# Kernel optimization log

Measured on AMD Instinct MI355X. Metric: run time of the kernel, lower is better.

The kernel has to match this reference:

```python
import jax, jax.numpy as jnp
import numpy as np

N_NODES = 10000
N_EDGES = 128000


def _edge_conv(x, row, col, edge_attr, w1, b1, w2, b2):
    # gather endpoints, concat edge features, 2-layer MLP per edge
    m = jnp.concatenate([x[row], x[col], edge_attr], axis=1)  # [E, 2*in+edge]
    m = jax.nn.relu(m @ w1 + b1) @ w2 + b2                    # [E, out]
    # scatter-mean onto source nodes (flow='target_to_source' -> aggregate on row)
    n = x.shape[0]
    s = jax.ops.segment_sum(m, row, num_segments=n)
    cnt = jax.ops.segment_sum(jnp.ones((row.shape[0], 1), m.dtype), row, num_segments=n)
    out = s / jnp.maximum(cnt, 1.0)
    return out, m


def setup_inputs() -> dict:
    key = jax.random.key(0)
    ks = jax.random.split(key, 24)
    f = jnp.float32

    def lin(kw, kb, fan_in, fan_out):
        lim = 1.0 / np.sqrt(fan_in)
        w = jax.random.uniform(kw, (fan_in, fan_out), f, -lim, lim)
        b = jax.random.uniform(kb, (fan_out,), f, -lim, lim)
        return w, b

    inp = {}
    inp['x_org'] = jax.random.normal(ks[0], (N_NODES, 256), f)
    inp['x_rot'] = jax.random.normal(ks[1], (N_NODES, 4), f)
    inp['edge_index'] = jax.random.randint(ks[2], (2, N_EDGES), 0, N_NODES, jnp.int64 if jax.config.jax_enable_x64 else jnp.int32)
    inp['edge_attr'] = jax.random.normal(ks[3], (N_EDGES, 640), f)
    inp['edge_rot'] = jax.random.normal(ks[4], (N_EDGES, 4), f)

    # conv1: Linear(2*260+644=1164, 64), Linear(64, 64)
    inp['c1_w1'], inp['c1_b1'] = lin(ks[5], ks[6], 1164, 64)
    inp['c1_w2'], inp['c1_b2'] = lin(ks[7], ks[8], 64, 64)
    # conv2: Linear(2*64+704=832, 64), Linear(64, 64)
    inp['c2_w1'], inp['c2_b1'] = lin(ks[9], ks[10], 832, 64)
    inp['c2_w2'], inp['c2_b2'] = lin(ks[11], ks[12], 64, 64)
    # conv3: Linear(2*128+128=384, 64), Linear(64, 64)
    inp['c3_w1'], inp['c3_b1'] = lin(ks[13], ks[14], 384, 64)
    inp['c3_w2'], inp['c3_b2'] = lin(ks[15], ks[16], 64, 64)
    # conv4: Linear(384, 64), Linear(64, 64)
    inp['c4_w1'], inp['c4_b1'] = lin(ks[17], ks[18], 384, 64)
    inp['c4_w2'], inp['c4_b2'] = lin(ks[19], ks[20], 64, 64)
    # lin1: Linear(64, 4)
    inp['lin1_w'], inp['lin1_b'] = lin(ks[21], ks[22], 64, 4)
    # edge_fc: Linear(64, 32) -> ReLU -> Linear(32, 1)
    k23 = jax.random.split(ks[23], 4)
    inp['efc_w1'], inp['efc_b1'] = lin(k23[0], k23[1], 64, 32)
    inp['efc_w2'], inp['efc_b2'] = lin(k23[2], k23[3], 32, 1)
    return inp


def reference(x_org, x_rot, edge_index, edge_attr, edge_rot,
              c1_w1, c1_b1, c1_w2, c1_b2,
              c2_w1, c2_b1, c2_w2, c2_b2,
              c3_w1, c3_b1, c3_w2, c3_b2,
              c4_w1, c4_b1, c4_w2, c4_b2,
              lin1_w, lin1_b, efc_w1, efc_b1, efc_w2, efc_b2):
    node_feat = jnp.concatenate([x_org, x_rot], axis=1)
    edge_feat = jnp.concatenate([edge_attr, edge_rot], axis=1)
    row, col = edge_index[0], edge_index[1]
    E = edge_index.shape[1]

    x1, edge_x1 = _edge_conv(node_feat, row, col, edge_feat, c1_w1, c1_b1, c1_w2, c1_b2)
    edge_x1 = jax.nn.relu(edge_x1)

    x2, edge_x2 = _edge_conv(x1, row, col, jnp.concatenate([edge_attr, edge_x1], axis=1),
                             c2_w1, c2_b1, c2_w2, c2_b2)
    x2 = jax.nn.relu(x2)
    edge_x2 = jax.nn.relu(edge_x2)

    x3, edge_x3 = _edge_conv(jnp.concatenate([x2, x1], axis=1), row, col,
                             jnp.concatenate([edge_x2, edge_x1], axis=1),
                             c3_w1, c3_b1, c3_w2, c3_b2)
    x3 = jax.nn.relu(x3)
    edge_x3 = jax.nn.relu(edge_x3)

    x4, edge_x4 = _edge_conv(jnp.concatenate([x3, x2], axis=1), row, col,
                             jnp.concatenate([edge_x3, edge_x2], axis=1),
                             c4_w1, c4_b1, c4_w2, c4_b2)
    x4 = jax.nn.relu(x4)

    x = x4 @ lin1_w + lin1_b  # [N, 4]
    h = edge_x4[: E // 2] + edge_x4[E // 2:]
    pred_edge_res = jax.nn.relu(h @ efc_w1 + efc_b1) @ efc_w2 + efc_b2  # [E/2, 1]

    # F.normalize(x, p=2, dim=1)
    x = x / jnp.maximum(jnp.linalg.norm(x, axis=1, keepdims=True), 1e-12)
    return x, pred_edge_res
```

## Files before the change

### kernel.cpp

```cpp
#include <hip/hip_runtime.h>
#include <stdint.h>


#define N_NODES 10000
#define N_EDGES 128000
#define E_HALF  64000
#define NBLK    1000

typedef unsigned short u16;

using bf16x8 = __attribute__((ext_vector_type(8))) short;
using f32x4  = __attribute__((ext_vector_type(4))) float;

#define MFMA16(A, B, C) C = __builtin_amdgcn_mfma_f32_16x16x32_bf16(A, B, C, 0, 0, 0)

__device__ __align__(256) float g_acc[N_NODES * 64];
__device__ __align__(256) float g_deg[N_NODES];
__device__ __align__(256) float g_P[N_NODES * 128];
__device__ __align__(256) float g_x1[N_NODES * 64];
__device__ __align__(256) float g_x2[N_NODES * 64];
__device__ __align__(256) float g_x3[N_NODES * 64];
__device__ __align__(256) u16  g_fragA[(size_t)NBLK * 16384];
__device__ __align__(256) u16  g_fragB[(size_t)NBLK * 16384];
__device__ __align__(256) float g_Q2 [(size_t)NBLK * 8192];
__device__ __align__(256) float g_ex4[(size_t)N_EDGES * 64];
__device__ __align__(256) u16  g_wpA_hi[5 * 4096];
__device__ __align__(256) u16  g_wpA_lo[5 * 4096];
__device__ __align__(256) u16  g_wp2_hi[4 * 4096];
__device__ __align__(256) u16  g_wp2_lo[4 * 4096];
__device__ __align__(256) u16  g_wnp_hi[9 * 8192];
__device__ __align__(256) u16  g_wnp_lo[9 * 8192];
__device__ __align__(256) u16  g_wpC_hi[10 * 8192];
__device__ __align__(256) u16  g_wpC_lo[10 * 8192];
__device__ __align__(256) int g_row[N_EDGES];
__device__ __align__(256) int g_col[N_EDGES];
__device__ int g_mode;
__device__ int g_is64;

__device__ __forceinline__ float b2f(u16 u) {
    return __uint_as_float(((unsigned int)u) << 16);
}
__device__ __forceinline__ u16 f2b(float f) {
    unsigned int u = __float_as_uint(f);
    u += 0x7FFFu + ((u >> 16) & 1u);
    return (u16)(u >> 16);
}
__device__ __forceinline__ float ldf(const u16* p)   { return b2f(*p); }
__device__ __forceinline__ float ldf(const float* p) { return *p; }
__device__ __forceinline__ void  stf(u16* p, float v)   { *p = f2b(v); }
__device__ __forceinline__ void  stf(float* p, float v) { *p = v; }

__device__ __forceinline__ float4 load4(const float* p) { return *(const float4*)p; }
__device__ __forceinline__ float4 load4(const u16* p) {
    ushort4 v = *(const ushort4*)p;
    return make_float4(b2f(v.x), b2f(v.y), b2f(v.z), b2f(v.w));
}

__device__ __forceinline__ void gl_lds16(const void* g, void* l) {
    __builtin_amdgcn_global_load_lds(
        (const __attribute__((address_space(1))) void*)g,
        (__attribute__((address_space(3))) void*)l, 16, 0, 0);
}

__device__ __forceinline__ void split_pack(float4 v, uint2& hi, uint2& lo) {
    unsigned int ux = __float_as_uint(v.x), uy = __float_as_uint(v.y);
    unsigned int uz = __float_as_uint(v.z), uw = __float_as_uint(v.w);
    unsigned int hx = ux & 0xFFFF0000u, hy = uy & 0xFFFF0000u;
    unsigned int hz = uz & 0xFFFF0000u, hw = uw & 0xFFFF0000u;
    hi.x = (hx >> 16) | hy;
    hi.y = (hz >> 16) | hw;
    u16 lx = f2b(v.x - __uint_as_float(hx));
    u16 ly = f2b(v.y - __uint_as_float(hy));
    u16 lz = f2b(v.z - __uint_as_float(hz));
    u16 lw = f2b(v.w - __uint_as_float(hw));
    lo.x = (unsigned int)lx | ((unsigned int)ly << 16);
    lo.y = (unsigned int)lz | ((unsigned int)lw << 16);
}

__device__ __forceinline__ void mk_frag(float4 v0, float4 v1,
                                        bf16x8& fh, bf16x8& fl) {
    uint2 h0, l0, h1, l1;
    split_pack(v0, h0, l0);
    split_pack(v1, h1, l1);
    union { unsigned int w[4]; bf16x8 v; } H, L;
    H.w[0] = h0.x; H.w[1] = h0.y; H.w[2] = h1.x; H.w[3] = h1.y;
    L.w[0] = l0.x; L.w[1] = l0.y; L.w[2] = l1.x; L.w[3] = l1.y;
    fh = H.v; fl = L.v;
}

__global__ void prologue_a(const void* x_org_v, const int* __restrict__ eidx) {
    const int i = blockIdx.x * 256 + threadIdx.x;
    g_acc[i] = 0.f;
    if (i < N_NODES) g_deg[i] = 0.f;
    if (blockIdx.x == 0 && threadIdx.x < 64) {
        const u16* w = (const u16*)x_org_v;
        const int t = threadIdx.x;
        int ok = 0;
        for (int j = t; j < 128; j += 64) {
            u16 v = w[j];
            int ex = (v >> 7) & 0xFF;
            ok += ((ex >= 0x68 && ex <= 0x88) || ((v & 0x7FFFu) == 0)) ? 1 : 0;
        }
        #pragma unroll
        for (int off = 32; off >= 1; off >>= 1) ok += __shfl_xor(ok, off);
        bool allz = true;
        for (int j = t; j < 2048; j += 64) allz = allz && (eidx[2 * j + 1] == 0);
        unsigned long long m = __ballot(allz);
        if (t == 0) {
            g_mode = (ok >= 110) ? 0 : 1;
            g_is64 = (m == ~0ull) ? 1 : 0;
        }
    }
}

__device__ __forceinline__ void pack_pair(u16* dh, u16* dl, float v) {
    const u16 hh = f2b(v);
    *dh = hh; *dl = f2b(v - b2f(hh));
}
template<typename TW>
__device__ void pack_wnp(const TW* w, int hioff, int rem, u16* dh, u16* dl) {
    const int s = rem >> 13, kt = (rem >> 12) & 1, ct = (rem >> 9) & 7,
              l = (rem >> 3) & 63, r = rem & 7;
    const int k = s * 64 + kt * 32 + 4 * (l >> 4) + (r & 3) + 16 * (r >> 2);
    const int col = ct * 16 + (l & 15);
    const int row = (col < 64) ? k : (hioff + k);
    pack_pair(dh + rem, dl + rem, ldf(w + (size_t)row * 64 + (col & 63)));
}
template<typename TW>
__device__ void pack_wpa(const TW* w, int we, int rem, u16* dh, u16* dl) {
    const int s = rem >> 12, kt = (rem >> 11) & 1, ct = (rem >> 9) & 3,
              l = (rem >> 3) & 63, r = rem & 7;
    const int k = s * 64 + kt * 32 + 4 * (l >> 4) + (r & 3) + 16 * (r >> 2);
    pack_pair(dh + rem, dl + rem,
              ldf(w + (size_t)(we + k) * 64 + ct * 16 + (l & 15)));
}
template<typename TW>
__device__ void pack_wpc(const TW* w1, const TW* w2w, int rem) {
    const int s = rem >> 13, kt = (rem >> 12) & 1, ct = (rem >> 9) & 7,
              l = (rem >> 3) & 63, r = rem & 7;
    const int k = s * 64 + kt * 32 + 4 * (l >> 4) + (r & 3) + 16 * (r >> 2);
    const int col = ct * 16 + (l & 15);
    float v = (col < 64) ? ldf(w1 + (size_t)(520 + k) * 64 + col)
                         : ldf(w2w + (size_t)(128 + k) * 64 + (col - 64));
    pack_pair(g_wpC_hi + rem, g_wpC_lo + rem, v);
}

template<typename TW>
__device__ void pack_all_body(const TW* c1w1, const TW* c1w2, const TW* c2w1,
        const TW* c2w2, const TW* c3w1, const TW* c3w2, const TW* c4w1,
        const TW* c4w2) {
    const int idx = blockIdx.x * 256 + threadIdx.x;
    if (idx < 81920)        pack_wpc<TW>(c1w1, c2w1, idx);
    else if (idx < 114688)  pack_wnp<TW>(c1w1, 260, idx - 81920,  g_wnp_hi,            g_wnp_lo);
    else if (idx < 122880)  pack_wnp<TW>(c2w1, 64,  idx - 114688, g_wnp_hi + 4 * 8192, g_wnp_lo + 4 * 8192);
    else if (idx < 139264)  pack_wnp<TW>(c3w1, 128, idx - 122880, g_wnp_hi + 5 * 8192, g_wnp_lo + 5 * 8192);
    else if (idx < 155648)  pack_wnp<TW>(c4w1, 128, idx - 139264, g_wnp_hi + 7 * 8192, g_wnp_lo + 7 * 8192);
    else if (idx < 159744)  pack_wpa<TW>(c2w1, 768, idx - 155648, g_wpA_hi,            g_wpA_lo);
    else if (idx < 167936)  pack_wpa<TW>(c3w1, 256, idx - 159744, g_wpA_hi + 4096,     g_wpA_lo + 4096);
    else if (idx < 176128)  pack_wpa<TW>(c4w1, 256, idx - 167936, g_wpA_hi + 12288,    g_wpA_lo + 12288);
    else if (idx < 180224)  pack_wpa<TW>(c1w2, 0,   idx - 176128, g_wp2_hi,            g_wp2_lo);
    else if (idx < 184320)  pack_wpa<TW>(c2w2, 0,   idx - 180224, g_wp2_hi + 4096,     g_wp2_lo + 4096);
    else if (idx < 188416)  pack_wpa<TW>(c3w2, 0,   idx - 184320, g_wp2_hi + 8192,     g_wp2_lo + 8192);
    else if (idx < 192512)  pack_wpa<TW>(c4w2, 0,   idx - 188416, g_wp2_hi + 12288,    g_wp2_lo + 12288);
}

__global__ void prep_k(const void* c1w1, const void* c1w2, const void* c2w1,
        const void* c2w2, const void* c3w1, const void* c3w2, const void* c4w1,
        const void* c4w2, const int* __restrict__ eidx) {
    if ((int)blockIdx.x < 752) {
        if (g_mode == 0)
            pack_all_body<u16>((const u16*)c1w1, (const u16*)c1w2, (const u16*)c2w1,
                (const u16*)c2w2, (const u16*)c3w1, (const u16*)c3w2,
                (const u16*)c4w1, (const u16*)c4w2);
        else
            pack_all_body<float>((const float*)c1w1, (const float*)c1w2,
                (const float*)c2w1, (const float*)c2w2, (const float*)c3w1,
                (const float*)c3w2, (const float*)c4w1, (const float*)c4w2);
    } else {
        const int e = ((int)blockIdx.x - 752) * 256 + threadIdx.x;
        int row, col;
        if (g_is64) { row = eidx[2 * e]; col = eidx[2 * (e + N_EDGES)]; }
        else        { row = eidx[e];     col = eidx[e + N_EDGES]; }
        g_row[e] = row; g_col[e] = col;
        atomicAdd(&g_deg[row], 1.0f);
    }
}

template<typename TA>
__device__ void node_mfma_in_body(float* smrot, float* smwt,
        const TA* A1, const TA* rotsrc, const TA* w1, float* P) {
    const int t = threadIdx.x;
    const int lane = t & 63, wid = t >> 6;
    const int q = lane >> 4, n = lane & 15;
    const int r0b = blockIdx.x * 64;

    if (t < 64) {
        const int rr = min(r0b + t, N_NODES - 1);
        float4 v = load4(rotsrc + (size_t)rr * 4);
        smrot[t * 4 + 0] = v.x; smrot[t * 4 + 1] = v.y;
        smrot[t * 4 + 2] = v.z; smrot[t * 4 + 3] = v.w;
    }
    for (int i = t; i < 512; i += 256) {
        const int j = i >> 7, c = i & 127;
        const int row = (c < 64) ? (256 + j) : (516 + j);
        smwt[i] = ldf(w1 + (size_t)row * 64 + (c & 63));
    }
    __syncthreads();

    const int arow = min(r0b + wid * 16 + n, N_NODES - 1);

    f32x4 acc[8];
    #pragma unroll
    for (int ct = 0; ct < 8; ++ct) acc[ct] = (f32x4){0.f, 0.f, 0.f, 0.f};

    #pragma unroll
    for (int s = 0; s < 4; ++s) {
        #pragma unroll
        for (int kt = 0; kt < 2; ++kt) {
            const TA* p = A1 + (size_t)arow * 256 + s * 64 + kt * 32 + q * 4;
            float4 v0 = load4(p), v1 = load4(p + 16);
            bf16x8 ah, al;
            mk_frag(v0, v1, ah, al);
            const u16* wph = g_wnp_hi + s * 8192;
            const u16* wpl = g_wnp_lo + s * 8192;
            #pragma unroll
            for (int ct = 0; ct < 8; ++ct) {
                bf16x8 bh = *(const bf16x8*)&wph[(kt * 8 + ct) * 512 + lane * 8];
                bf16x8 bl = *(const bf16x8*)&wpl[(kt * 8 + ct) * 512 + lane * 8];
                MFMA16(ah, bh, acc[ct]);
                MFMA16(al, bh, acc[ct]);
                MFMA16(ah, bl, acc[ct]);
            }
        }
    }

    #pragma unroll
    for (int ct = 0; ct < 8; ++ct) {
        #pragma unroll
        for (int i = 0; i < 4; ++i) {
            const int rl = wid * 16 + 4 * q + i;
            const int row = r0b + rl;
            const int col = ct * 16 + n;
            float v = acc[ct][i]
                    + smrot[rl * 4 + 0] * smwt[0 * 128 + col]
                    + smrot[rl * 4 + 1] * smwt[1 * 128 + col]
                    + smrot[rl * 4 + 2] * smwt[2 * 128 + col]
                    + smrot[rl * 4 + 3] * smwt[3 * 128 + col];
            if (row < N_NODES) P[(size_t)row * 128 + col] = v;
        }
    }
}

__global__ void __launch_bounds__(256) node_mfma_in(
        const void* A1, const void* rotsrc, const void* w1, float* __restrict__ P) {
    __shared__ float smrot[256], smwt[512];
    if (g_mode == 0)
        node_mfma_in_body<u16>(smrot, smwt, (const u16*)A1, (const u16*)rotsrc,
                               (const u16*)w1, P);
    else
        node_mfma_in_body<float>(smrot, smwt, (const float*)A1, (const float*)rotsrc,
                               (const float*)w1, P);
}

template<int NS2, bool RELU>
__global__ void __launch_bounds__(256) node_mfma_acc(
        const float* A2, float* __restrict__ xout, float* __restrict__ P,
        int wnpoff) {
    const int t = threadIdx.x;
    const int lane = t & 63, wid = t >> 6;
    const int q = lane >> 4, n = lane & 15;
    const int r0b = blockIdx.x * 64;
    const int rown = r0b + wid * 16 + n;
    const int arow = min(rown, N_NODES - 1);
    const bool own = rown < N_NODES;
    const float inv = 1.0f / fmaxf(g_deg[arow], 1.0f);

    f32x4 acc[8];
    #pragma unroll
    for (int ct = 0; ct < 8; ++ct) acc[ct] = (f32x4){0.f, 0.f, 0.f, 0.f};

    #pragma unroll
    for (int kt = 0; kt < 2; ++kt) {
        float* p = g_acc + (size_t)arow * 64 + kt * 32 + q * 4;
        float4 v0 = load4(p), v1 = load4(p + 16);
        v0.x *= inv; v0.y *= inv; v0.z *= inv; v0.w *= inv;
        v1.x *= inv; v1.y *= inv; v1.z *= inv; v1.w *= inv;
        if (RELU) {
            v0.x = fmaxf(v0.x, 0.f); v0.y = fmaxf(v0.y, 0.f);
            v0.z = fmaxf(v0.z, 0.f); v0.w = fmaxf(v0.w, 0.f);
            v1.x = fmaxf(v1.x, 0.f); v1.y = fmaxf(v1.y, 0.f);
            v1.z = fmaxf(v1.z, 0.f); v1.w = fmaxf(v1.w, 0.f);
        }
        if (own) {
            *(float4*)(xout + (size_t)arow * 64 + kt * 32 + q * 4) = v0;
            *(float4*)(xout + (size_t)arow * 64 + kt * 32 + q * 4 + 16) = v1;
            *(float4*)p = make_float4(0.f, 0.f, 0.f, 0.f);
            *(float4*)(p + 16) = make_float4(0.f, 0.f, 0.f, 0.f);
        }
        bf16x8 ah, al;
        mk_frag(v0, v1, ah, al);
        const u16* wph = g_wnp_hi + wnpoff;
        const u16* wpl = g_wnp_lo + wnpoff;
        #pragma unroll
        for (int ct = 0; ct < 8; ++ct) {
            bf16x8 bh = *(const bf16x8*)&wph[(kt * 8 + ct) * 512 + lane * 8];
            bf16x8 bl = *(const bf16x8*)&wpl[(kt * 8 + ct) * 512 + lane * 8];
            MFMA16(ah, bh, acc[ct]);
            MFMA16(al, bh, acc[ct]);
            MFMA16(ah, bl, acc[ct]);
        }
    }
    if constexpr (NS2 > 0) {
        #pragma unroll
        for (int kt = 0; kt < 2; ++kt) {
            const float* p = A2 + (size_t)arow * 64 + kt * 32 + q * 4;
            float4 v0 = load4(p), v1 = load4(p + 16);
            bf16x8 ah, al;
            mk_frag(v0, v1, ah, al);
            const u16* wph = g_wnp_hi + wnpoff + 8192;
            const u16* wpl = g_wnp_lo + wnpoff + 8192;
            #pragma unroll
            for (int ct = 0; ct < 8; ++ct) {
                bf16x8 bh = *(const bf16x8*)&wph[(kt * 8 + ct) * 512 + lane * 8];
                bf16x8 bl = *(const bf16x8*)&wpl[(kt * 8 + ct) * 512 + lane * 8];
                MFMA16(ah, bh, acc[ct]);
                MFMA16(al, bh, acc[ct]);
                MFMA16(ah, bl, acc[ct]);
            }
        }
    }

    #pragma unroll
    for (int ct = 0; ct < 8; ++ct) {
        #pragma unroll
        for (int i = 0; i < 4; ++i) {
            const int rl = wid * 16 + 4 * q + i;
            const int row = r0b + rl;
            if (row < N_NODES) P[(size_t)row * 128 + ct * 16 + n] = acc[ct][i];
        }
    }
}

__device__ __forceinline__ void frag_store_o(u16* hreg, int wid, int lane,
        const f32x4 (&oacc)[2][4], u16* Fdst, int blkid) {
    const int q = lane >> 4, n = lane & 15;
    #pragma unroll
    for (int rt = 0; rt < 2; ++rt)
        #pragma unroll
        for (int ct = 0; ct < 4; ++ct)
            #pragma unroll
            for (int i = 0; i < 4; ++i) {
                float v = fmaxf(oacc[rt][ct][i], 0.f);
                unsigned int hb = __float_as_uint(v) & 0xFFFF0000u;
                const u16 hh = (u16)(hb >> 16);
                const u16 hl = f2b(v - __uint_as_float(hb));
                const int off = wid * 4096
                              + (((ct >> 1) * 2 + rt) * 64 + (n >> 2) * 16 + 4 * q + i) * 8
                              + (ct & 1) * 4 + (n & 3);
                hreg[off]        = hh;
                hreg[off + 2048] = hl;
            }
    #pragma unroll
    for (int kt = 0; kt < 2; ++kt)
        #pragma unroll
        for (int rtl = 0; rtl < 2; ++rtl) {
            const int src = wid * 4096 + ((kt * 2 + rtl) * 64 + lane) * 8;
            bf16x8 h8 = *(const bf16x8*)&hreg[src];
            bf16x8 l8 = *(const bf16x8*)&hreg[src + 2048];
            const size_t gb = (size_t)blkid * 16384
                            + (size_t)(kt * 8 + wid * 2 + rtl) * 512 + lane * 8;
            *(bf16x8*)&Fdst[gb]        = h8;
            *(bf16x8*)&Fdst[gb + 8192] = l8;
        }
}

template<typename TA, typename TW>
__device__ void edge_c1_body(u16* smW, int* srow, int* scol,
        float* b1s, float* b2s, float* rot, float* wtl,
        const TA* efa, const TA* rotsrc,
        const TW* w1, const TW* b1v, const TW* b2v) {
    const int t = threadIdx.x;
    const int lane = t & 63, wid = t >> 6;
    const int q = lane >> 4, n = lane & 15;
    const int e0 = blockIdx.x * 128;

    #pragma unroll
    for (int i = 0; i < 4; ++i) {
        const int L = wid * 4096 + i * 1024;
        const char* src = (L < 8192) ? (const char*)g_wp2_hi + L
                                     : (const char*)g_wp2_lo + (L - 8192);
        gl_lds16(src + lane * 16, (char*)smW + 49152 + L);
    }

    if (t < 128) srow[t] = g_row[e0 + t];
    else         scol[t - 128] = g_col[e0 + t - 128];
    if (t >= 128 && t < 192) b1s[t - 128] = ldf(b1v + (t - 128));
    if (t >= 192)            b2s[t - 192] = ldf(b2v + (t - 192));
    if (t < 128) {
        float4 r4 = load4(rotsrc + (size_t)(e0 + t) * 4);
        rot[t * 4 + 0] = r4.x; rot[t * 4 + 1] = r4.y;
        rot[t * 4 + 2] = r4.z; rot[t * 4 + 3] = r4.w;
    }
    wtl[t] = ldf(w1 + (size_t)(1160 + (t >> 6)) * 64 + (t & 63));

    const TA* arow0 = efa + (size_t)(e0 + wid * 32 + n) * 640;
    const TA* arow1 = efa + (size_t)(e0 + wid * 32 + 16 + n) * 640;

    f32x4 acc[2][8];
    #pragma unroll
    for (int a_ = 0; a_ < 2; ++a_)
        #pragma unroll
        for (int b_ = 0; b_ < 8; ++b_)
            acc[a_][b_] = (f32x4){0.f, 0.f, 0.f, 0.f};

    auto stageW = [&](int h, int bufbyte) {
        const char* sh = (const char*)g_wpC_hi + (size_t)h * 8192;
        const char* sl = (const char*)g_wpC_lo + (size_t)h * 8192;
        char* d = (char*)smW + bufbyte;
        #pragma unroll
        for (int i = 0; i < 2; ++i) {
            const int off = wid * 2048 + i * 1024;
            gl_lds16(sh + off + lane * 16, d + off);
            gl_lds16(sl + off + lane * 16, d + 8192 + off);
        }
    };
    auto issueA = [&](float4 (&buf)[2][2], int h) {
        const int cb = (h >> 1) * 64 + (h & 1) * 32 + q * 4;
        buf[0][0] = load4(arow0 + cb);
        buf[0][1] = load4(arow0 + cb + 16);
        buf[1][0] = load4(arow1 + cb);
        buf[1][1] = load4(arow1 + cb + 16);
    };
    auto step = [&](float4 (&buf)[2][2], int wb_u16) {
        bf16x8 ah0, al0, ah1, al1;
        mk_frag(buf[0][0], buf[0][1], ah0, al0);
        mk_frag(buf[1][0], buf[1][1], ah1, al1);
        #pragma unroll
        for (int ct = 0; ct < 8; ++ct) {
            bf16x8 bh = *(const bf16x8*)&smW[wb_u16 + ct * 512 + lane * 8];
            bf16x8 bl = *(const bf16x8*)&smW[wb_u16 + 4096 + ct * 512 + lane * 8];
            MFMA16(ah0, bh, acc[0][ct]);
            MFMA16(ah1, bh, acc[1][ct]);
            MFMA16(al0, bh, acc[0][ct]);
            MFMA16(al1, bh, acc[1][ct]);
            MFMA16(ah0, bl, acc[0][ct]);
            MFMA16(ah1, bl, acc[1][ct]);
        }
    };

    float4 a0[2][2], a1[2][2], a2[2][2], a3[2][2];

    stageW(0, 0);
    issueA(a0, 0);
    issueA(a1, 1);
    __builtin_amdgcn_sched_barrier(0);
    asm volatile("s_waitcnt vmcnt(12) lgkmcnt(0)");
    __builtin_amdgcn_sched_barrier(0);
    __builtin_amdgcn_s_barrier();

#define C1B(H, AC, AN, VM)                                                    \
    do {                                                                      \
        if constexpr ((H) < 19) stageW((H) + 1, (((H) + 1) % 3) * 16384);     \
        if constexpr ((H) < 18) issueA(AN, (H) + 2);                          \
        __builtin_amdgcn_sched_barrier(0);                                    \
        asm volatile("s_waitcnt vmcnt(" VM ")");                              \
        __builtin_amdgcn_sched_barrier(0);                                    \
        __builtin_amdgcn_s_barrier();                                         \
        __builtin_amdgcn_s_setprio(1);                                        \
        step(AC, ((H) % 3) * 8192);                                           \
        __builtin_amdgcn_s_setprio(0);                                        \
    } while (0)

    C1B(0,  a0, a2, "12"); C1B(1,  a1, a3, "12");
    C1B(2,  a2, a0, "12"); C1B(3,  a3, a1, "12");
    C1B(4,  a0, a2, "12"); C1B(5,  a1, a3, "12");
    C1B(6,  a2, a0, "12"); C1B(7,  a3, a1, "12");
    C1B(8,  a0, a2, "12"); C1B(9,  a1, a3, "12");
    C1B(10, a2, a0, "12"); C1B(11, a3, a1, "12");
    C1B(12, a0, a2, "12"); C1B(13, a1, a3, "12");
    C1B(14, a2, a0, "12"); C1B(15, a3, a1, "12");
    C1B(16, a0, a2, "12"); C1B(17, a1, a3, "12");
    C1B(18, a2, a0, "8");  C1B(19, a3, a1, "0");
#undef C1B

    __builtin_amdgcn_s_barrier();

    {
        float* qf = g_Q2 + (size_t)blockIdx.x * 8192 + (size_t)t * 32;
        #pragma unroll
        for (int rt = 0; rt < 2; ++rt)
            #pragma unroll
            for (int c2 = 0; c2 < 4; ++c2)
                *(f32x4*)(qf + rt * 16 + c2 * 4) = acc[rt][4 + c2];
    }

    u16* hreg = smW;
    #pragma unroll
    for (int rt = 0; rt < 2; ++rt)
        #pragma unroll
        for (int ct = 0; ct < 4; ++ct)
            #pragma unroll
            for (int i = 0; i < 4; ++i) {
                const int rl = wid * 32 + rt * 16 + 4 * q + i;
                const int col = ct * 16 + n;
                float v = acc[rt][ct][i] + b1s[col]
                        + g_P[(size_t)srow[rl] * 128 + col]
                        + g_P[(size_t)scol[rl] * 128 + 64 + col]
                        + rot[rl * 4 + 0] * wtl[0 * 64 + col]
                        + rot[rl * 4 + 1] * wtl[1 * 64 + col]
                        + rot[rl * 4 + 2] * wtl[2 * 64 + col]
                        + rot[rl * 4 + 3] * wtl[3 * 64 + col];
                v = fmaxf(v, 0.f);
                unsigned int hb = __float_as_uint(v) & 0xFFFF0000u;
                const u16 hh = (u16)(hb >> 16);
                const u16 hl = f2b(v - __uint_as_float(hb));
                const int off = wid * 4096
                              + (((ct >> 1) * 2 + rt) * 64 + (n >> 2) * 16 + 4 * q + i) * 8
                              + (ct & 1) * 4 + (n & 3);
                hreg[off]        = hh;
                hreg[off + 2048] = hl;
            }

    f32x4 oacc[2][4];
    #pragma unroll
    for (int rt = 0; rt < 2; ++rt)
        #pragma unroll
        for (int ct = 0; ct < 4; ++ct) {
            const float bb = b2s[ct * 16 + n];
            oacc[rt][ct] = (f32x4){bb, bb, bb, bb};
        }
    #pragma unroll
    for (int kt = 0; kt < 2; ++kt) {
        const int r0 = wid * 4096 + ((kt * 2 + 0) * 64 + lane) * 8;
        const int r1 = wid * 4096 + ((kt * 2 + 1) * 64 + lane) * 8;
        bf16x8 ah0 = *(const bf16x8*)&hreg[r0];
        bf16x8 ah1 = *(const bf16x8*)&hreg[r1];
        bf16x8 al0 = *(const bf16x8*)&hreg[r0 + 2048];
        bf16x8 al1 = *(const bf16x8*)&hreg[r1 + 2048];
        #pragma unroll
        for (int ct = 0; ct < 4; ++ct) {
            bf16x8 bh = *(const bf16x8*)&smW[24576 + (kt * 4 + ct) * 512 + lane * 8];
            bf16x8 bl = *(const bf16x8*)&smW[28672 + (kt * 4 + ct) * 512 + lane * 8];
            MFMA16(ah0, bh, oacc[0][ct]);
            MFMA16(ah1, bh, oacc[1][ct]);
            MFMA16(al0, bh, oacc[0][ct]);
            MFMA16(al1, bh, oacc[1][ct]);
            MFMA16(ah0, bl, oacc[0][ct]);
            MFMA16(ah1, bl, oacc[1][ct]);
        }
    }

    #pragma unroll
    for (int rt = 0; rt < 2; ++rt)
        #pragma unroll
        for (int ct = 0; ct < 4; ++ct)
            #pragma unroll
            for (int i = 0; i < 4; ++i) {
                const int rl = wid * 32 + rt * 16 + 4 * q + i;
                atomicAdd(&g_acc[(size_t)srow[rl] * 64 + ct * 16 + n], oacc[rt][ct][i]);
            }
    frag_store_o(hreg, wid, lane, oacc, g_fragA, blockIdx.x);
}

__global__ void __launch_bounds__(256, 2) edge_c1(
        const void* efa, const void* rotsrc,
        const void* w1, const void* b1, const void* b2) {
    __shared__ __align__(16) u16 smW[32768];
    __shared__ int srow[128], scol[128];
    __shared__ float b1s[64], b2s[64], rot[512], wtl[256];
    if (g_mode == 0)
        edge_c1_body<u16, u16>(smW, srow, scol, b1s, b2s, rot, wtl,
            (const u16*)efa, (const u16*)rotsrc,
            (const u16*)w1, (const u16*)b1, (const u16*)b2);
    else
        edge_c1_body<float, float>(smW, srow, scol, b1s, b2s, rot, wtl,
            (const float*)efa, (const float*)rotsrc,
            (const float*)w1, (const float*)b1, (const float*)b2);
}

template<typename TW, int NSF, bool HASQ2, bool FRAG_OUT>
__device__ void edge_lite_body(u16* smW, int* srow, int* scol,
        float* b1s, float* b2s,
        const u16* f0, const u16* f1,
        const TW* b1v, const TW* b2v, u16* Ffrag, float* fout,
        int wpAoff, int wp2off) {
    const int t = threadIdx.x;
    const int lane = t & 63, wid = t >> 6;
    const int q = lane >> 4, n = lane & 15;
    const int e0 = blockIdx.x * 128;
    const size_t blkb = (size_t)blockIdx.x * 16384;
    constexpr int N2 = 16384;

    #pragma unroll
    for (int i = 0; i < (NSF + 1) * 4; ++i) {
        const int j = i * 4 + wid;
        const char* src;
        int dstB;
        if (j < NSF * 8) {
            src = (const char*)(g_wpA_hi + wpAoff) + j * 1024;            dstB = j * 1024;
        } else if (j < NSF * 16) {
            src = (const char*)(g_wpA_lo + wpAoff) + (j - NSF * 8) * 1024; dstB = j * 1024;
        } else if (j < NSF * 16 + 8) {
            src = (const char*)(g_wp2_hi + wp2off) + (j - NSF * 16) * 1024;
            dstB = 32768 + (j - NSF * 16) * 1024;
        } else {
            src = (const char*)(g_wp2_lo + wp2off) + (j - NSF * 16 - 8) * 1024;
            dstB = 32768 + (j - NSF * 16) * 1024;
        }
        gl_lds16(src + lane * 16, (char*)smW + dstB);
    }

    if (t < 128) srow[t] = g_row[e0 + t];
    else         scol[t - 128] = g_col[e0 + t - 128];
    if (t >= 128 && t < 192) b1s[t - 128] = ldf(b1v + (t - 128));
    if (t >= 192)            b2s[t - 192] = ldf(b2v + (t - 192));
    __syncthreads();

    float pr[2][4][4], pc[2][4][4];
    #pragma unroll
    for (int rt = 0; rt < 2; ++rt)
        #pragma unroll
        for (int ct = 0; ct < 4; ++ct)
            #pragma unroll
            for (int i = 0; i < 4; ++i) {
                const int rl = wid * 32 + rt * 16 + 4 * q + i;
                const int col = ct * 16 + n;
                pr[rt][ct][i] = g_P[(size_t)srow[rl] * 128 + col];
                pc[rt][ct][i] = g_P[(size_t)scol[rl] * 128 + 64 + col];
            }

    f32x4 acc[2][4];
    #pragma unroll
    for (int a_ = 0; a_ < 2; ++a_)
        #pragma unroll
        for (int b_ = 0; b_ < 4; ++b_)
            acc[a_][b_] = (f32x4){0.f, 0.f, 0.f, 0.f};

    #pragma unroll
    for (int s = 0; s < NSF; ++s) {
        const u16* fs = (s == 0) ? f0 : f1;
        #pragma unroll
        for (int kt = 0; kt < 2; ++kt) {
            const size_t ba0 = blkb + (size_t)(kt * 8 + wid * 2 + 0) * 512 + lane * 8;
            const size_t ba1 = blkb + (size_t)(kt * 8 + wid * 2 + 1) * 512 + lane * 8;
            bf16x8 ah0 = *(const bf16x8*)&fs[ba0];
            bf16x8 al0 = *(const bf16x8*)&fs[ba0 + 8192];
            bf16x8 ah1 = *(const bf16x8*)&fs[ba1];
            bf16x8 al1 = *(const bf16x8*)&fs[ba1 + 8192];
            #pragma unroll
            for (int ct = 0; ct < 4; ++ct) {
                bf16x8 bh = *(const bf16x8*)&smW[s * 4096 + (kt * 4 + ct) * 512 + lane * 8];
                bf16x8 bl = *(const bf16x8*)&smW[NSF * 4096 + s * 4096 + (kt * 4 + ct) * 512 + lane * 8];
                MFMA16(ah0, bh, acc[0][ct]);
                MFMA16(ah1, bh, acc[1][ct]);
                MFMA16(al0, bh, acc[0][ct]);
                MFMA16(al1, bh, acc[1][ct]);
                MFMA16(ah0, bl, acc[0][ct]);
                MFMA16(ah1, bl, acc[1][ct]);
            }
        }
    }

    __builtin_amdgcn_s_barrier();
    u16* hreg = smW;

    const float* qf = g_Q2 + (size_t)blockIdx.x * 8192 + (size_t)t * 32;
    #pragma unroll
    for (int rt = 0; rt < 2; ++rt)
        #pragma unroll
        for (int ct = 0; ct < 4; ++ct) {
            f32x4 qv;
            if constexpr (HASQ2) qv = *(const f32x4*)(qf + rt * 16 + ct * 4);
            #pragma unroll
            for (int i = 0; i < 4; ++i) {
                const int rl = wid * 32 + rt * 16 + 4 * q + i;
                const int col = ct * 16 + n;
                float v = acc[rt][ct][i] + b1s[col]
                        + pr[rt][ct][i] + pc[rt][ct][i];
                if constexpr (HASQ2) v += qv[i];
                v = fmaxf(v, 0.f);
                unsigned int hb = __float_as_uint(v) & 0xFFFF0000u;
                const u16 hh = (u16)(hb >> 16);
                const u16 hl = f2b(v - __uint_as_float(hb));
                const int off = wid * 4096
                              + (((ct >> 1) * 2 + rt) * 64 + (n >> 2) * 16 + 4 * q + i) * 8
                              + (ct & 1) * 4 + (n & 3);
                hreg[off]        = hh;
                hreg[off + 2048] = hl;
            }
        }

    f32x4 oacc[2][4];
    #pragma unroll
    for (int rt = 0; rt < 2; ++rt)
        #pragma unroll
        for (int ct = 0; ct < 4; ++ct) {
            const float bb = b2s[ct * 16 + n];
            oacc[rt][ct] = (f32x4){bb, bb, bb, bb};
        }
    #pragma unroll
    for (int kt = 0; kt < 2; ++kt) {
        const int r0 = wid * 4096 + ((kt * 2 + 0) * 64 + lane) * 8;
        const int r1 = wid * 4096 + ((kt * 2 + 1) * 64 + lane) * 8;
        bf16x8 ah0 = *(const bf16x8*)&hreg[r0];
        bf16x8 ah1 = *(const bf16x8*)&hreg[r1];
        bf16x8 al0 = *(const bf16x8*)&hreg[r0 + 2048];
        bf16x8 al1 = *(const bf16x8*)&hreg[r1 + 2048];
        #pragma unroll
        for (int ct = 0; ct < 4; ++ct) {
            bf16x8 bh = *(const bf16x8*)&smW[N2 + (kt * 4 + ct) * 512 + lane * 8];
            bf16x8 bl = *(const bf16x8*)&smW[N2 + 4096 + (kt * 4 + ct) * 512 + lane * 8];
            MFMA16(ah0, bh, oacc[0][ct]);
            MFMA16(ah1, bh, oacc[1][ct]);
            MFMA16(al0, bh, oacc[0][ct]);
            MFMA16(al1, bh, oacc[1][ct]);
            MFMA16(ah0, bl, oacc[0][ct]);
            MFMA16(ah1, bl, oacc[1][ct]);
        }
    }

    #pragma unroll
    for (int rt = 0; rt < 2; ++rt)
        #pragma unroll
        for (int ct = 0; ct < 4; ++ct)
            #pragma unroll
            for (int i = 0; i < 4; ++i) {
                const int rl = wid * 32 + rt * 16 + 4 * q + i;
                const int col = ct * 16 + n;
                const float v = oacc[rt][ct][i];
                atomicAdd(&g_acc[(size_t)srow[rl] * 64 + col], v);
                if constexpr (!FRAG_OUT)
                    fout[(size_t)(e0 + rl) * 64 + col] = v;
            }
    if constexpr (FRAG_OUT)
        frag_store_o(hreg, wid, lane, oacc, Ffrag, blockIdx.x);
}

template<int NSF, bool HASQ2, bool FRAG_OUT>
__global__ void __launch_bounds__(256, 3) edge_lite(
        const u16* f0, const u16* f1, const void* b1, const void* b2,
        u16* Ffrag, float* fout, int wpAoff, int wp2off) {
    __shared__ __align__(16) u16 smW[24576];
    __shared__ int srow[128], scol[128];
    __shared__ float b1s[64], b2s[64];
    if (g_mode == 0)
        edge_lite_body<u16, NSF, HASQ2, FRAG_OUT>(smW, srow, scol, b1s, b2s,
            f0, f1, (const u16*)b1, (const u16*)b2, Ffrag, fout, wpAoff, wp2off);
    else
        edge_lite_body<float, NSF, HASQ2, FRAG_OUT>(smW, srow, scol, b1s, b2s,
            f0, f1, (const float*)b1, (const float*)b2, Ffrag, fout, wpAoff, wp2off);
}

template<typename T>
__device__ void final_node_body(const T* w, const T* b, T* out, int bid) {
    const int t = threadIdx.x;
    const int lane = t & 63;
    const int n = bid * 4 + (t >> 6);
    float inv = 1.0f / fmaxf(g_deg[n], 1.0f);
    float x4 = fmaxf(g_acc[(size_t)n * 64 + lane] * inv, 0.0f);
    float r[4];
    #pragma unroll
    for (int j = 0; j < 4; ++j) {
        float v = x4 * ldf(w + lane * 4 + j);
        #pragma unroll
        for (int off = 32; off >= 1; off >>= 1) v += __shfl_xor(v, off);
        r[j] = v + ldf(b + j);
    }
    float nrm = sqrtf(r[0]*r[0] + r[1]*r[1] + r[2]*r[2] + r[3]*r[3]);
    float dn = fmaxf(nrm, 1e-12f);
    if (lane < 4) stf(out + n * 4 + lane, r[lane] / dn);
}

template<typename T>
__device__ void edge_head_body(const float* ex4, const T* w1, const T* b1,
                               const T* w2, const T* b2, T* out, int bid) {
    __shared__ float lw1[2048];
    __shared__ float lw2[32];
    const int t = threadIdx.x;
    for (int i = t; i < 2048; i += 256) lw1[i] = ldf(w1 + i);
    if (t < 32) lw2[t] = ldf(w2 + t);
    __syncthreads();
    const int e = bid * 256 + t;
    float a[32];
    #pragma unroll
    for (int j = 0; j < 32; ++j) a[j] = ldf(b1 + j);
    const float* p0 = ex4 + (size_t)e * 64;
    const float* p1 = ex4 + (size_t)(e + E_HALF) * 64;
    for (int c = 0; c < 64; ++c) {
        float h = p0[c] + p1[c];
        #pragma unroll
        for (int j = 0; j < 32; ++j) a[j] += h * lw1[c * 32 + j];
    }
    float s = ldf(b2);
    #pragma unroll
    for (int j = 0; j < 32; ++j) s += fmaxf(a[j], 0.f) * lw2[j];
    stf(out + e, s);
}

__global__ void __launch_bounds__(256) tail_k(
        const void* lw, const void* lb, const float* ex4,
        const void* ew1, const void* eb1, const void* ew2, const void* eb2,
        void* out) {
    const int b = blockIdx.x;
    if (b < 2500) {
        if (g_mode == 0) final_node_body<u16>((const u16*)lw, (const u16*)lb, (u16*)out, b);
        else             final_node_body<float>((const float*)lw, (const float*)lb, (float*)out, b);
    } else {
        if (g_mode == 0)
            edge_head_body<u16>(ex4, (const u16*)ew1, (const u16*)eb1,
                (const u16*)ew2, (const u16*)eb2, (u16*)out + 40000, b - 2500);
        else
            edge_head_body<float>(ex4, (const float*)ew1, (const float*)eb1,
                (const float*)ew2, (const float*)eb2, (float*)out + 40000, b - 2500);
    }
}

__global__ void sentinel_fill(unsigned int* out, int n_words) {
    int i = blockIdx.x * 256 + threadIdx.x;
    if (i < n_words) out[i] = 0x44794479u;
}

static void* sym_addr(const void* symbol) {
    void* p = nullptr;
    (void)hipGetSymbolAddress(&p, symbol);
    return p;
}

extern "C" void kernel_launch(void* const* d_in, const int* in_sizes, int n_in,
                              void* d_out, int out_size, void* d_ws, size_t ws_size,
                              hipStream_t stream) {
    (void)d_ws; (void)ws_size;
    bool ok = (n_in == 27) && (out_size == 104000)
           && (in_sizes[0] == 2560000) && (in_sizes[2] == 256000)
           && (in_sizes[3] == 81920000) && (in_sizes[5] == 74496)
           && (in_sizes[21] == 256) && (in_sizes[25] == 32);
    if (!ok) {
        sentinel_fill<<<204, 256, 0, stream>>>((unsigned int*)d_out, 52000);
        return;
    }
    const void* x_org     = d_in[0];
    const void* x_rot     = d_in[1];
    const int*  eidx      = (const int*)d_in[2];
    const void* edge_attr = d_in[3];
    const void* edge_rot  = d_in[4];

    float* P   = (float*)sym_addr(HIP_SYMBOL(g_P));
    float* x1  = (float*)sym_addr(HIP_SYMBOL(g_x1));
    float* x2  = (float*)sym_addr(HIP_SYMBOL(g_x2));
    float* x3  = (float*)sym_addr(HIP_SYMBOL(g_x3));
    u16*   fA  = (u16*)sym_addr(HIP_SYMBOL(g_fragA));
    u16*   fB  = (u16*)sym_addr(HIP_SYMBOL(g_fragB));
    float* ex4 = (float*)sym_addr(HIP_SYMBOL(g_ex4));

    prologue_a<<<2500, 256, 0, stream>>>(x_org, eidx);
    prep_k<<<1252, 256, 0, stream>>>(d_in[5], d_in[7], d_in[9], d_in[11],
                                     d_in[13], d_in[15], d_in[17], d_in[19], eidx);

    node_mfma_in<<<157, 256, 0, stream>>>(x_org, x_rot, d_in[5], P);
    edge_c1<<<NBLK, 256, 0, stream>>>(edge_attr, edge_rot, d_in[5], d_in[6], d_in[8]);

    node_mfma_acc<0, false><<<157, 256, 0, stream>>>(nullptr, x1, P, 4 * 8192);
    edge_lite<1, true, true><<<NBLK, 256, 0, stream>>>(
        fA, nullptr, d_in[10], d_in[12], fB, nullptr, 0, 4096);

    node_mfma_acc<1, true><<<157, 256, 0, stream>>>(x1, x2, P, 5 * 8192);
    edge_lite<2, false, true><<<NBLK, 256, 0, stream>>>(
        fB, fA, d_in[14], d_in[16], fA, nullptr, 4096, 8192);
    node_mfma_acc<1, true><<<157, 256, 0, stream>>>(x2, x3, P, 7 * 8192);
    edge_lite<2, false, false><<<NBLK, 256, 0, stream>>>(
        fA, fB, d_in[18], d_in[20], nullptr, ex4, 12288, 12288);

    tail_k<<<2750, 256, 0, stream>>>(d_in[21], d_in[22], ex4,
                                     d_in[23], d_in[24], d_in[25], d_in[26], d_out);
}
```

Before: 801.1 us.

## Double edge_c1 block to 512 threads sharing staged weight tiles

The first edge-conv kernel now runs 500 blocks of 512 threads (256 edges each) instead of 1000 blocks of 256, so each staged weight chunk in LDS is shared by twice as many edges. Each wave issues half as many global-to-LDS copies per stage, and the vmcnt waits are adjusted to match. The second-layer weights are no longer staged into LDS and are read straight from global memory. Per-block outputs are remapped to the original 128-edge fragment layout. Risks include higher register and LDS pressure with launch_bounds(512,4), and uncached global reads for the second-layer weights.

```diff
diff --git a/kernel.cpp b/kernel.cpp
--- a/kernel.cpp
+++ b/kernel.cpp
@@ -374,6 +374,40 @@
         }
 }
 
+__device__ __forceinline__ void frag_store_o2(u16* hreg, int wid, int lane,
+        const f32x4 (&oacc)[2][4], u16* Fdst, int blkid2x) {
+    const int q = lane >> 4, n = lane & 15;
+    const int widc = wid & 3;
+    #pragma unroll
+    for (int rt = 0; rt < 2; ++rt)
+        #pragma unroll
+        for (int ct = 0; ct < 4; ++ct)
+            #pragma unroll
+            for (int i = 0; i < 4; ++i) {
+                float v = fmaxf(oacc[rt][ct][i], 0.f);
+                unsigned int hb = __float_as_uint(v) & 0xFFFF0000u;
+                const u16 hh = (u16)(hb >> 16);
+                const u16 hl = f2b(v - __uint_as_float(hb));
+                const int off = wid * 4096
+                              + (((ct >> 1) * 2 + rt) * 64 + (n >> 2) * 16 + 4 * q + i) * 8
+                              + (ct & 1) * 4 + (n & 3);
+                hreg[off]        = hh;
+                hreg[off + 2048] = hl;
+            }
+    #pragma unroll
+    for (int kt = 0; kt < 2; ++kt)
+        #pragma unroll
+        for (int rtl = 0; rtl < 2; ++rtl) {
+            const int src = wid * 4096 + ((kt * 2 + rtl) * 64 + lane) * 8;
+            bf16x8 h8 = *(const bf16x8*)&hreg[src];
+            bf16x8 l8 = *(const bf16x8*)&hreg[src + 2048];
+            const size_t gb = (size_t)blkid2x * 16384
+                            + (size_t)(kt * 8 + widc * 2 + rtl) * 512 + lane * 8;
+            *(bf16x8*)&Fdst[gb]        = h8;
+            *(bf16x8*)&Fdst[gb + 8192] = l8;
+        }
+}
+
 template<typename TA, typename TW>
 __device__ void edge_c1_body(u16* smW, int* srow, int* scol,
         float* b1s, float* b2s, float* rot, float* wtl,
@@ -382,26 +416,18 @@
     const int t = threadIdx.x;
     const int lane = t & 63, wid = t >> 6;
     const int q = lane >> 4, n = lane & 15;
-    const int e0 = blockIdx.x * 128;
-
-    #pragma unroll
-    for (int i = 0; i < 4; ++i) {
-        const int L = wid * 4096 + i * 1024;
-        const char* src = (L < 8192) ? (const char*)g_wp2_hi + L
-                                     : (const char*)g_wp2_lo + (L - 8192);
-        gl_lds16(src + lane * 16, (char*)smW + 49152 + L);
-    }
-
-    if (t < 128) srow[t] = g_row[e0 + t];
-    else         scol[t - 128] = g_col[e0 + t - 128];
-    if (t >= 128 && t < 192) b1s[t - 128] = ldf(b1v + (t - 128));
-    if (t >= 192)            b2s[t - 192] = ldf(b2v + (t - 192));
-    if (t < 128) {
+    const int e0 = blockIdx.x * 256;
+
+    if (t < 256) srow[t] = g_row[e0 + t];
+    else         scol[t - 256] = g_col[e0 + t - 256];
+    if (t < 64)            b1s[t] = ldf(b1v + t);
+    else if (t < 128)      b2s[t - 64] = ldf(b2v + (t - 64));
+    if (t < 256) {
         float4 r4 = load4(rotsrc + (size_t)(e0 + t) * 4);
         rot[t * 4 + 0] = r4.x; rot[t * 4 + 1] = r4.y;
         rot[t * 4 + 2] = r4.z; rot[t * 4 + 3] = r4.w;
-    }
-    wtl[t] = ldf(w1 + (size_t)(1160 + (t >> 6)) * 64 + (t & 63));
+        wtl[t] = ldf(w1 + (size_t)(1160 + (t >> 6)) * 64 + (t & 63));
+    }
 
     const TA* arow0 = efa + (size_t)(e0 + wid * 32 + n) * 640;
     const TA* arow1 = efa + (size_t)(e0 + wid * 32 + 16 + n) * 640;
@@ -417,12 +443,9 @@
         const char* sh = (const char*)g_wpC_hi + (size_t)h * 8192;
         const char* sl = (const char*)g_wpC_lo + (size_t)h * 8192;
         char* d = (char*)smW + bufbyte;
-        #pragma unroll
-        for (int i = 0; i < 2; ++i) {
-            const int off = wid * 2048 + i * 1024;
-            gl_lds16(sh + off + lane * 16, d + off);
-            gl_lds16(sl + off + lane * 16, d + 8192 + off);
-        }
+        const int off = wid * 1024;
+        gl_lds16(sh + off + lane * 16, d + off);
+        gl_lds16(sl + off + lane * 16, d + 8192 + off);
     };
     auto issueA = [&](float4 (&buf)[2][2], int h) {
         const int cb = (h >> 1) * 64 + (h & 1) * 32 + q * 4;
@@ -454,7 +477,7 @@
     issueA(a0, 0);
     issueA(a1, 1);
     __builtin_amdgcn_sched_barrier(0);
-    asm volatile("s_waitcnt vmcnt(12) lgkmcnt(0)");
+    asm volatile("s_waitcnt vmcnt(10) lgkmcnt(0)");
     __builtin_amdgcn_sched_barrier(0);
     __builtin_amdgcn_s_barrier();
 
@@ -471,22 +494,23 @@
         __builtin_amdgcn_s_setprio(0);                                        \
     } while (0)
 
-    C1B(0,  a0, a2, "12"); C1B(1,  a1, a3, "12");
-    C1B(2,  a2, a0, "12"); C1B(3,  a3, a1, "12");
-    C1B(4,  a0, a2, "12"); C1B(5,  a1, a3, "12");
-    C1B(6,  a2, a0, "12"); C1B(7,  a3, a1, "12");
-    C1B(8,  a0, a2, "12"); C1B(9,  a1, a3, "12");
-    C1B(10, a2, a0, "12"); C1B(11, a3, a1, "12");
-    C1B(12, a0, a2, "12"); C1B(13, a1, a3, "12");
-    C1B(14, a2, a0, "12"); C1B(15, a3, a1, "12");
-    C1B(16, a0, a2, "12"); C1B(17, a1, a3, "12");
-    C1B(18, a2, a0, "8");  C1B(19, a3, a1, "0");
+    C1B(0,  a0, a2, "10"); C1B(1,  a1, a3, "10");
+    C1B(2,  a2, a0, "10"); C1B(3,  a3, a1, "10");
+    C1B(4,  a0, a2, "10"); C1B(5,  a1, a3, "10");
+    C1B(6,  a2, a0, "10"); C1B(7,  a3, a1, "10");
+    C1B(8,  a0, a2, "10"); C1B(9,  a1, a3, "10");
+    C1B(10, a2, a0, "10"); C1B(11, a3, a1, "10");
+    C1B(12, a0, a2, "10"); C1B(13, a1, a3, "10");
+    C1B(14, a2, a0, "10"); C1B(15, a3, a1, "10");
+    C1B(16, a0, a2, "10"); C1B(17, a1, a3, "10");
+    C1B(18, a2, a0, "6");  C1B(19, a3, a1, "0");
 #undef C1B
 
     __builtin_amdgcn_s_barrier();
 
     {
-        float* qf = g_Q2 + (size_t)blockIdx.x * 8192 + (size_t)t * 32;
+        const int cb2 = blockIdx.x * 2 + (wid >> 2);
+        float* qf = g_Q2 + (size_t)cb2 * 8192 + (size_t)(t & 255) * 32;
         #pragma unroll
         for (int rt = 0; rt < 2; ++rt)
             #pragma unroll
@@ -539,8 +563,8 @@
         bf16x8 al1 = *(const bf16x8*)&hreg[r1 + 2048];
         #pragma unroll
         for (int ct = 0; ct < 4; ++ct) {
-            bf16x8 bh = *(const bf16x8*)&smW[24576 + (kt * 4 + ct) * 512 + lane * 8];
-            bf16x8 bl = *(const bf16x8*)&smW[28672 + (kt * 4 + ct) * 512 + lane * 8];
+            bf16x8 bh = *(const bf16x8*)&g_wp2_hi[(kt * 4 + ct) * 512 + lane * 8];
+            bf16x8 bl = *(const bf16x8*)&g_wp2_lo[(kt * 4 + ct) * 512 + lane * 8];
             MFMA16(ah0, bh, oacc[0][ct]);
             MFMA16(ah1, bh, oacc[1][ct]);
             MFMA16(al0, bh, oacc[0][ct]);
@@ -559,15 +583,15 @@
                 const int rl = wid * 32 + rt * 16 + 4 * q + i;
                 atomicAdd(&g_acc[(size_t)srow[rl] * 64 + ct * 16 + n], oacc[rt][ct][i]);
             }
-    frag_store_o(hreg, wid, lane, oacc, g_fragA, blockIdx.x);
-}
-
-__global__ void __launch_bounds__(256, 2) edge_c1(
+    frag_store_o2(hreg, wid, lane, oacc, g_fragA, blockIdx.x * 2 + (wid >> 2));
+}
+
+__global__ void __launch_bounds__(512, 4) edge_c1(
         const void* efa, const void* rotsrc,
         const void* w1, const void* b1, const void* b2) {
     __shared__ __align__(16) u16 smW[32768];
-    __shared__ int srow[128], scol[128];
-    __shared__ float b1s[64], b2s[64], rot[512], wtl[256];
+    __shared__ int srow[256], scol[256];
+    __shared__ float b1s[64], b2s[64], rot[1024], wtl[256];
     if (g_mode == 0)
         edge_c1_body<u16, u16>(smW, srow, scol, b1s, b2s, rot, wtl,
             (const u16*)efa, (const u16*)rotsrc,
@@ -857,7 +881,7 @@
                                      d_in[13], d_in[15], d_in[17], d_in[19], eidx);
 
     node_mfma_in<<<157, 256, 0, stream>>>(x_org, x_rot, d_in[5], P);
-    edge_c1<<<NBLK, 256, 0, stream>>>(edge_attr, edge_rot, d_in[5], d_in[6], d_in[8]);
+    edge_c1<<<500, 512, 0, stream>>>(edge_attr, edge_rot, d_in[5], d_in[6], d_in[8]);
 
     node_mfma_acc<0, false><<<157, 256, 0, stream>>>(nullptr, x1, P, 4 * 8192);
     edge_lite<1, true, true><<<NBLK, 256, 0, stream>>>(
```

New measurement: 914.0 us. 14.1% more time.
